# Performance work log

Hardware: AMD Instinct MI355X
Metric: run time of the kernel (lower is better)

The kernel has to match this reference:

```python
import jax, jax.numpy as jnp
import numpy as np
from jax import lax

SIM_THRESH = 0.9
MOTION_SCALE = 0.5
SALIENCY_SCALE = 0.5
EPS = 1e-6


def setup_inputs() -> dict:
    key = jax.random.key(0)
    k1, k2, k3, k4 = jax.random.split(key, 4)
    B, N, D, H, W = 128, 196, 768, 14, 14
    return {
        "tokens": jax.random.normal(k1, (B, N, D), dtype=jnp.float32),
        "motion_magnitude": jax.random.uniform(k2, (B, 1, H, W), dtype=jnp.float32),
        "saliency_map": jax.random.uniform(k3, (B, 1, H, W), dtype=jnp.float32),
        "compression_ratio": jax.random.uniform(k4, (B, H, W), dtype=jnp.float32),
    }


def _importance(motion, saliency, ratio):
    # motion/saliency are already (B,1,14,14) == (height,width), so
    # adaptive_avg_pool2d to (14,14) is the identity.
    B = motion.shape[0]
    m = motion.reshape(B, -1)
    m = m / (jnp.max(m) + EPS)               # global max, as in torch .max()
    s = saliency.reshape(B, -1)
    s = s / (jnp.max(s) + EPS)
    r = ratio.reshape(B, -1)
    imp = (MOTION_SCALE * m + SALIENCY_SCALE * s
           + (1.0 - MOTION_SCALE - SALIENCY_SCALE) * r)
    lo = imp.min(axis=1, keepdims=True)
    hi = imp.max(axis=1, keepdims=True)
    return (imp - lo) / (hi - lo + EPS)      # (B, N)


def _groups(adj):
    """Sequential BFS grouping over roots, faithful to the torch loop.

    adj: bool (N,N) directed edge mask. Returns (group_ids int32 (N,), num_groups).
    """
    N = adj.shape[0]

    def root_step(carry, r):
        assigned, gids, gid = carry

        def assign(c):
            assigned, gids, gid = c
            # BFS from root r, only through currently-unassigned nodes
            allowed = (~assigned).at[r].set(True)
            reach0 = jnp.zeros(N, dtype=bool).at[r].set(True)

            def body(s):
                reach, _ = s
                nxt = reach | (jnp.any(adj & reach[:, None], axis=0) & allowed)
                return nxt, jnp.any(nxt != reach)

            reach, _ = lax.while_loop(lambda s: s[1], body, (reach0, True))
            return assigned | reach, jnp.where(reach, gid, gids), gid + 1

        carry = lax.cond(assigned[r], lambda c: c, assign, carry)
        return carry, None

    init = (jnp.zeros(N, dtype=bool), jnp.zeros(N, dtype=jnp.int32), jnp.int32(0))
    (_, gids, ngroups), _ = lax.scan(root_step, init, jnp.arange(N))
    return gids, ngroups


def _merge_one(tokens_b, imp_b, adj_b):
    N = tokens_b.shape[0]
    gids, ng = _groups(adj_b)
    denom = jax.ops.segment_sum(imp_b, gids, num_segments=N) + EPS
    w = imp_b / denom[gids]
    merged = jax.ops.segment_sum(tokens_b * w[:, None], gids, num_segments=N)
    return merged, gids, ng


def reference(tokens, motion_magnitude, saliency_map, compression_ratio):
    B, N, D = tokens.shape
    imp = _importance(motion_magnitude, saliency_map, compression_ratio)  # (B,N)

    # cosine similarity (F.normalize with eps=1e-12)
    norm = jnp.maximum(jnp.linalg.norm(tokens, axis=-1, keepdims=True), 1e-12)
    tn = tokens / norm
    sim = jnp.einsum('bnd,bmd->bnm', tn, tn)
    sim = sim * (1.0 - jnp.eye(N, dtype=sim.dtype))  # zero diagonal

    # directed merge mask: similarity * (1 - importance_row)
    mask = (sim > SIM_THRESH).astype(sim.dtype) * (1.0 - imp[:, :, None])
    adj = mask > 0.5

    merged, gids, ng = jax.vmap(_merge_one)(tokens, imp, adj)
    # merged padded to N groups (rows >= num_groups are zero)
    return merged, sim, imp, gids
```

## Files before the change

kernel.cpp:

```cpp
#include <hip/hip_runtime.h>
#include <cstdint>

static constexpr int cB = 128;
static constexpr int cN = 196;
static constexpr int cD = 768;
static constexpr int cNN = cN * cN;
static constexpr int cND = cN * cD;
static constexpr float cEPS = 1e-6f;
static constexpr size_t cBND = (size_t)cB * cN * cD;

typedef __attribute__((ext_vector_type(8))) short short8;
typedef __attribute__((ext_vector_type(8))) unsigned short u16x8;
typedef __attribute__((ext_vector_type(4))) float f32x4;
typedef unsigned long long u64;

__device__ __forceinline__ unsigned short bf16_rne(float x) {
    unsigned u = __builtin_bit_cast(unsigned, x);
    u += 0x7FFFu + ((u >> 16) & 1u);
    return (unsigned short)(u >> 16);
}

__global__ __launch_bounds__(256) void k_imp(const float* __restrict__ mo,
                                             const float* __restrict__ sa,
                                             float* __restrict__ out_imp,
                                             float* __restrict__ ws_imp,
                                             float* __restrict__ ws_w,
                                             u64* __restrict__ ws_adj) {
    int b = blockIdx.x, t = threadIdx.x;
    __shared__ float redm[4], reds[4], lo_s[4], hi_s[4], MS[2], LOHI[2];

    for (int i = b * 256 + t; i < cB * cN * 4; i += cB * 256) ws_adj[i] = 0ull;

    const float4* mo4 = (const float4*)mo;
    const float4* sa4 = (const float4*)sa;
    float mm = 0.f, ms = 0.f;
    for (int i = t; i < cB * cN / 4; i += 256) {
        float4 a = mo4[i], c = sa4[i];
        mm = fmaxf(mm, fmaxf(fmaxf(a.x, a.y), fmaxf(a.z, a.w)));
        ms = fmaxf(ms, fmaxf(fmaxf(c.x, c.y), fmaxf(c.z, c.w)));
    }
    #pragma unroll
    for (int off = 32; off; off >>= 1) {
        mm = fmaxf(mm, __shfl_down(mm, off));
        ms = fmaxf(ms, __shfl_down(ms, off));
    }
    if ((t & 63) == 0) { redm[t >> 6] = mm; reds[t >> 6] = ms; }
    __syncthreads();
    if (t == 0) {
        float a = redm[0], c = reds[0];
        for (int w = 1; w < 4; w++) { a = fmaxf(a, redm[w]); c = fmaxf(c, reds[w]); }
        MS[0] = 1.0f / (a + cEPS);
        MS[1] = 1.0f / (c + cEPS);
    }
    __syncthreads();
    float Minv = MS[0], Sinv = MS[1];
    float v = 0.f, lo = 1e30f, hi = -1e30f;
    if (t < cN) {
        v = 0.5f * mo[b * cN + t] * Minv + 0.5f * sa[b * cN + t] * Sinv;
        lo = v; hi = v;
    }
    #pragma unroll
    for (int off = 32; off; off >>= 1) {
        lo = fminf(lo, __shfl_down(lo, off));
        hi = fmaxf(hi, __shfl_down(hi, off));
    }
    if ((t & 63) == 0) { lo_s[t >> 6] = lo; hi_s[t >> 6] = hi; }
    __syncthreads();
    if (t == 0) {
        float l = lo_s[0], h = hi_s[0];
        for (int w = 1; w < 4; w++) { l = fminf(l, lo_s[w]); h = fmaxf(h, hi_s[w]); }
        LOHI[0] = l; LOHI[1] = h;
    }
    __syncthreads();
    if (t < cN) {
        float imp = (v - LOHI[0]) / (LOHI[1] - LOHI[0] + cEPS);
        out_imp[b * cN + t] = imp;
        ws_imp[b * cN + t] = imp;
        ws_w[b * cN + t] = imp / (imp + cEPS);
    }
}

__global__ __launch_bounds__(256) void k_prep(const float* __restrict__ tok,
                                              const float* __restrict__ ws_w,
                                              float* __restrict__ ws_invn,
                                              float* __restrict__ merged) {
    int t = threadIdx.x;
    int tk = blockIdx.x * 8 + (t >> 5);
    int l  = t & 31;
    const float4* src = (const float4*)(tok + (size_t)tk * cD) + l;
    float4* dst = (float4*)(merged + (size_t)tk * cD) + l;
    float w = ws_w[tk];
    float4 v[6];
    #pragma unroll
    for (int j = 0; j < 6; j++) v[j] = src[32 * j];
    float s = 0.f;
    #pragma unroll
    for (int j = 0; j < 6; j++) {
        float4 x = v[j];
        s += x.x * x.x + x.y * x.y + x.z * x.z + x.w * x.w;
        dst[32 * j] = make_float4(x.x * w, x.y * w, x.z * w, x.w * w);
    }
    s += __shfl_xor(s, 1);  s += __shfl_xor(s, 2);
    s += __shfl_xor(s, 4);  s += __shfl_xor(s, 8);
    s += __shfl_xor(s, 16);
    if (l == 0) ws_invn[tk] = 1.0f / fmaxf(sqrtf(s), 1e-12f);
}

__global__ __launch_bounds__(256, 2) void k_sim(const float* __restrict__ tok,
                                                const float* __restrict__ ws_invn,
                                                const float* __restrict__ ws_imp,
                                                float* __restrict__ out_sim,
                                                u64* __restrict__ ws_adj) {
    __shared__ unsigned short sA[128 * 40];
    __shared__ unsigned short sB[128 * 40];
    __shared__ float invR[128], invC[128], impR[128], impC[128];
    __shared__ u64 ldsAdj[256];
    __shared__ u64 ldsAdjT[256];

    int bid = blockIdx.x;
    int xcd = bid & 7;
    int lin = bid >> 3;
    int b   = xcd + 8 * (lin / 3);
    int tc  = lin % 3;
    int rb = (tc == 2) ? 128 : 0;
    int cb = (tc == 0) ? 0 : 128;
    bool diag = (tc != 1);

    int t = threadIdx.x;
    int w = t >> 6, lane = t & 63;
    int lr = lane & 15, kf = (lane >> 4) * 8;
    int wr = (w >> 1) * 64, wc = (w & 1) * 64;
    const size_t bN = (size_t)b * cN;
    const float* tb = tok + bN * cD;

    ldsAdj[t] = 0ull;
    ldsAdjT[t] = 0ull;
    if (t < 128) {
        int gr = rb + t;
        invR[t] = (gr < cN) ? ws_invn[bN + gr] : 0.f;
        impR[t] = (gr < cN) ? ws_imp[bN + gr] : 1.f;
    } else {
        int gc = cb + (t - 128);
        invC[t - 128] = (gc < cN) ? ws_invn[bN + gc] : 0.f;
        impC[t - 128] = (gc < cN) ? ws_imp[bN + gc] : 1.f;
    }

    f32x4 acc[4][4];
    #pragma unroll
    for (int i = 0; i < 4; i++)
        #pragma unroll
        for (int j = 0; j < 4; j++) acc[i][j] = (f32x4){0.f, 0.f, 0.f, 0.f};

    int srow = t >> 2;
    int q = t & 3;

    float4 bufA[8], bufB[8];

    auto LOADS = [&](int k0, float4 (&r)[8]) {
        int koff = k0 + 8 * q;
        #pragma unroll
        for (int p = 0; p < 2; ++p) {
            int row = srow + 64 * p;
            float4 z = make_float4(0.f, 0.f, 0.f, 0.f);
            r[2 * p] = z; r[2 * p + 1] = z;
            int gr = rb + row;
            if (gr < cN) {
                const float4* pa = (const float4*)(tb + (size_t)gr * cD + koff);
                r[2 * p] = pa[0]; r[2 * p + 1] = pa[1];
            }
            if (!diag) {
                r[4 + 2 * p] = z; r[4 + 2 * p + 1] = z;
                int gc = cb + row;
                if (gc < cN) {
                    const float4* pb = (const float4*)(tb + (size_t)gc * cD + koff);
                    r[4 + 2 * p] = pb[0]; r[4 + 2 * p + 1] = pb[1];
                }
            }
        }
    };
    auto PACK = [&](const float4 (&r)[8]) {
        #pragma unroll
        for (int p = 0; p < 2; ++p) {
            int row = srow + 64 * p;
            float4 a0 = r[2 * p], a1 = r[2 * p + 1];
            u16x8 ha;
            ha[0] = bf16_rne(a0.x); ha[1] = bf16_rne(a0.y);
            ha[2] = bf16_rne(a0.z); ha[3] = bf16_rne(a0.w);
            ha[4] = bf16_rne(a1.x); ha[5] = bf16_rne(a1.y);
            ha[6] = bf16_rne(a1.z); ha[7] = bf16_rne(a1.w);
            *(u16x8*)&sA[row * 40 + 8 * q] = ha;
            if (!diag) {
                float4 b0 = r[4 + 2 * p], b1 = r[4 + 2 * p + 1];
                u16x8 hb;
                hb[0] = bf16_rne(b0.x); hb[1] = bf16_rne(b0.y);
                hb[2] = bf16_rne(b0.z); hb[3] = bf16_rne(b0.w);
                hb[4] = bf16_rne(b1.x); hb[5] = bf16_rne(b1.y);
                hb[6] = bf16_rne(b1.z); hb[7] = bf16_rne(b1.w);
                *(u16x8*)&sB[row * 40 + 8 * q] = hb;
            }
        }
    };
    auto COMPUTE = [&]() {
        short8 af[4], bf[4];
        #pragma unroll
        for (int rg = 0; rg < 4; rg++)
            af[rg] = *(const short8*)&sA[(wr + 16 * rg + lr) * 40 + kf];
        const unsigned short* sS = diag ? sA : sB;
        #pragma unroll
        for (int cg = 0; cg < 4; cg++)
            bf[cg] = *(const short8*)&sS[(wc + 16 * cg + lr) * 40 + kf];
        #pragma unroll
        for (int rg = 0; rg < 4; rg++)
            #pragma unroll
            for (int cg = 0; cg < 4; cg++)
                acc[rg][cg] = __builtin_amdgcn_mfma_f32_16x16x32_bf16(
                    af[rg], bf[cg], acc[rg][cg], 0, 0, 0);
    };

    LOADS(0, bufA);
    for (int k0 = 0; k0 < cD; k0 += 64) {
        PACK(bufA);
        __syncthreads();
        LOADS(k0 + 32, bufB);
        COMPUTE();
        __syncthreads();

        PACK(bufB);
        __syncthreads();
        if (k0 + 64 < cD) LOADS(k0 + 64, bufA);
        COMPUTE();
        __syncthreads();
    }

    float* so = out_sim + (size_t)b * cNN;
    int wloc = w >> 1;
    #pragma unroll
    for (int rg = 0; rg < 4; rg++) {
        int rBaseLoc = wr + 16 * rg + (lane >> 4) * 4;
        #pragma unroll
        for (int cg = 0; cg < 4; cg++) {
            int cLoc = wc + 16 * cg + lr;
            int C = cb + cLoc;
            if (C >= cN) continue;
            float ic = invC[cLoc];
            float imC = impC[cLoc];
            u64 bits = 0ull;
            #pragma unroll
            for (int i = 0; i < 4; i++) {
                int rLoc = rBaseLoc + i;
                int R = rb + rLoc;
                if (R >= cN) continue;
                float val = (R == C) ? 0.f : acc[rg][cg][i] * invR[rLoc] * ic;
                so[(size_t)R * cN + C] = val;
                if (val > 0.9f && impR[rLoc] < 0.5f) bits |= 1ull << (R & 63);
                if (!diag) {
                    so[(size_t)C * cN + R] = val;
                    if (val > 0.9f && imC < 0.5f)
                        atomicOr(&ldsAdjT[rLoc * 2 + ((C >> 6) & 1)],
                                 1ull << (C & 63));
                }
            }
            if (bits) atomicOr(&ldsAdj[cLoc * 2 + wloc], bits);
        }
    }
    __syncthreads();
    {
        int cLoc = t >> 1, wl = t & 1;
        int C = cb + cLoc;
        u64 v = ldsAdj[t];
        if (C < cN && v)
            atomicOr(&ws_adj[((size_t)b * cN + C) * 4 + (rb >> 6) + wl], v);
        if (!diag) {
            u64 vt = ldsAdjT[t];
            if (vt)
                atomicOr(&ws_adj[((size_t)b * cN + cLoc) * 4 + 2 + wl], vt);
        }
    }
}

__global__ __launch_bounds__(256) void k_group(const u64* __restrict__ ws_adj,
                                               const float* __restrict__ ws_imp,
                                               const float* __restrict__ tok,
                                               float* __restrict__ out_gids,
                                               float* __restrict__ ws_w,
                                               int* __restrict__ ws_flag,
                                               int* __restrict__ ws_gids,
                                               float* __restrict__ merged) {
    int b = blockIdx.x, t = threadIdx.x;
    __shared__ float impL[cN];
    __shared__ u64 reachw[4], assignedw[4], edge_s[4];
    __shared__ int flag;
    __shared__ int gidsL[cN];
    __shared__ float denomL[cN];
    __shared__ float wL[cN];

    u64 m0 = 0, m1 = 0, m2 = 0, m3 = 0;
    if (t < cN) {
        impL[t] = ws_imp[b * cN + t];
        const u64* ap = ws_adj + ((size_t)b * cN + t) * 4;
        m0 = ap[0]; m1 = ap[1]; m2 = ap[2]; m3 = ap[3];
    }
    u64 anym = m0 | m1 | m2 | m3;
    u64 bal = __ballot(anym != 0ull);
    if ((t & 63) == 0) edge_s[t >> 6] = bal;
    __syncthreads();
    bool has_edges = (edge_s[0] | edge_s[1] | edge_s[2] | edge_s[3]) != 0ull;

    if (!has_edges) {
        if (t < cN) {
            float imp = impL[t];
            ws_w[b * cN + t] = imp / (imp + cEPS);
            ws_gids[b * cN + t] = t;
            out_gids[b * cN + t] = (float)t;
        }
        if (t == 0) ws_flag[b] = 1;
        return;
    }

    if (t < 4) assignedw[t] = 0ull;
    if (t < cN) { gidsL[t] = 0; denomL[t] = 0.f; }
    __syncthreads();
    int gid = 0;
    int wrd_t = t >> 6, bit_t = t & 63;
    for (int r = 0; r < cN; r++) {
        if ((assignedw[r >> 6] >> (r & 63)) & 1ull) continue;
        if (t < 4) reachw[t] = (t == (r >> 6)) ? (1ull << (r & 63)) : 0ull;
        __syncthreads();
        int changed = 1;
        while (changed) {
            u64 hit = (m0 & reachw[0]) | (m1 & reachw[1]) |
                      (m2 & reachw[2]) | (m3 & reachw[3]);
            bool inre = (t < cN) && ((reachw[wrd_t] >> bit_t) & 1ull);
            bool unass = (t < cN) && !((assignedw[wrd_t] >> bit_t) & 1ull);
            bool p = inre || (hit != 0ull && unass);
            u64 nw = __ballot(p);
            __syncthreads();
            if (t == 0) flag = 0;
            __syncthreads();
            if ((t & 63) == 0) {
                if (nw != reachw[t >> 6]) flag = 1;
                reachw[t >> 6] = nw;
            }
            __syncthreads();
            changed = flag;
        }
        if ((t < cN) && ((reachw[wrd_t] >> bit_t) & 1ull)) gidsL[t] = gid;
        if (t < 4) assignedw[t] |= reachw[t];
        gid++;
        __syncthreads();
    }
    if (t < cN) atomicAdd(&denomL[gidsL[t]], impL[t]);
    __syncthreads();
    if (t < cN) {
        int g = gidsL[t];
        float wv = impL[t] / (denomL[g] + cEPS);
        ws_w[b * cN + t] = wv;
        wL[t] = wv;
        ws_gids[b * cN + t] = g;
        out_gids[b * cN + t] = (float)g;
    }
    if (t == 0) ws_flag[b] = 0;
    __syncthreads();

    if (t < 192) {
        for (int n = 0; n < cN; n++) {
            float4 acc = make_float4(0.f, 0.f, 0.f, 0.f);
            for (int j = 0; j < cN; j++) {
                if (gidsL[j] == n) {
                    const float4 v = *(const float4*)(tok + (size_t)b * cND + (size_t)j * cD + 4 * t);
                    float wv = wL[j];
                    acc.x += v.x * wv; acc.y += v.y * wv;
                    acc.z += v.z * wv; acc.w += v.w * wv;
                }
            }
            *(float4*)(merged + (size_t)b * cND + (size_t)n * cD + 4 * t) = acc;
        }
    }
}

extern "C" void kernel_launch(void* const* d_in, const int* in_sizes, int n_in,
                              void* d_out, int out_size, void* d_ws, size_t ws_size,
                              hipStream_t stream) {
    const float* tok = (const float*)d_in[0];
    const float* mo  = (const float*)d_in[1];
    const float* sa  = (const float*)d_in[2];

    float* out = (float*)d_out;
    float* out_merged = out;
    float* out_sim    = out + cBND;
    float* out_imp    = out_sim + (size_t)cB * cNN;
    float* out_gids   = out_imp + (size_t)cB * cN;

    u64*   ws_adj  = (u64*)d_ws;
    float* ws_imp  = (float*)(ws_adj + (size_t)cB * cN * 4);
    float* ws_w    = ws_imp + cB * cN;
    float* ws_invn = ws_w + cB * cN;
    int*   ws_flag = (int*)(ws_invn + cB * cN);
    int*   ws_gids = ws_flag + cB;

    k_imp<<<cB, 256, 0, stream>>>(mo, sa, out_imp, ws_imp, ws_w, ws_adj);
    k_prep<<<cB * cN / 8, 256, 0, stream>>>(tok, ws_w, ws_invn, out_merged);
    k_sim<<<384, 256, 0, stream>>>(tok, ws_invn, ws_imp, out_sim, ws_adj);
    k_group<<<cB, 256, 0, stream>>>(ws_adj, ws_imp, tok, out_gids, ws_w,
                                    ws_flag, ws_gids, out_merged);
}
```

Measured before the change: 212.5 us.

## Fuse norm computation and merged-token init into similarity kernel

Removes the separate k_prep kernel. Its work of computing per-token inverse norms and writing the weighted token copy into merged now happens inside k_sim's PACK stage, using the fp32 values already loaded for the bf16 GEMM tiles. The diagonal tiles write merged rows and reduce the squared sums with shuffles and shared memory before the epilogue. This saves one full read of the tokens tensor and one launch, but adds stores and an extra sync to the GEMM kernel, which could slow its pipeline.

```diff
diff --git a/kernel.cpp b/kernel.cpp
--- a/kernel.cpp
+++ b/kernel.cpp
@@ -80,37 +80,12 @@
     }
 }
 
-__global__ __launch_bounds__(256) void k_prep(const float* __restrict__ tok,
-                                              const float* __restrict__ ws_w,
-                                              float* __restrict__ ws_invn,
-                                              float* __restrict__ merged) {
-    int t = threadIdx.x;
-    int tk = blockIdx.x * 8 + (t >> 5);
-    int l  = t & 31;
-    const float4* src = (const float4*)(tok + (size_t)tk * cD) + l;
-    float4* dst = (float4*)(merged + (size_t)tk * cD) + l;
-    float w = ws_w[tk];
-    float4 v[6];
-    #pragma unroll
-    for (int j = 0; j < 6; j++) v[j] = src[32 * j];
-    float s = 0.f;
-    #pragma unroll
-    for (int j = 0; j < 6; j++) {
-        float4 x = v[j];
-        s += x.x * x.x + x.y * x.y + x.z * x.z + x.w * x.w;
-        dst[32 * j] = make_float4(x.x * w, x.y * w, x.z * w, x.w * w);
-    }
-    s += __shfl_xor(s, 1);  s += __shfl_xor(s, 2);
-    s += __shfl_xor(s, 4);  s += __shfl_xor(s, 8);
-    s += __shfl_xor(s, 16);
-    if (l == 0) ws_invn[tk] = 1.0f / fmaxf(sqrtf(s), 1e-12f);
-}
-
 __global__ __launch_bounds__(256, 2) void k_sim(const float* __restrict__ tok,
-                                                const float* __restrict__ ws_invn,
+                                                const float* __restrict__ ws_w,
                                                 const float* __restrict__ ws_imp,
                                                 float* __restrict__ out_sim,
-                                                u64* __restrict__ ws_adj) {
+                                                u64* __restrict__ ws_adj,
+                                                float* __restrict__ merged) {
     __shared__ unsigned short sA[128 * 40];
     __shared__ unsigned short sB[128 * 40];
     __shared__ float invR[128], invC[128], impR[128], impC[128];
@@ -132,16 +107,15 @@
     int wr = (w >> 1) * 64, wc = (w & 1) * 64;
     const size_t bN = (size_t)b * cN;
     const float* tb = tok + bN * cD;
+    float* mg = merged + bN * cD;
 
     ldsAdj[t] = 0ull;
     ldsAdjT[t] = 0ull;
     if (t < 128) {
         int gr = rb + t;
-        invR[t] = (gr < cN) ? ws_invn[bN + gr] : 0.f;
         impR[t] = (gr < cN) ? ws_imp[bN + gr] : 1.f;
     } else {
         int gc = cb + (t - 128);
-        invC[t - 128] = (gc < cN) ? ws_invn[bN + gc] : 0.f;
         impC[t - 128] = (gc < cN) ? ws_imp[bN + gc] : 1.f;
     }
 
@@ -153,6 +127,14 @@
 
     int srow = t >> 2;
     int q = t & 3;
+
+    float wA0 = 0.f, wA1 = 0.f;
+    if (diag) {
+        int g0 = rb + srow, g1 = rb + srow + 64;
+        if (g0 < cN) wA0 = ws_w[bN + g0];
+        if (g1 < cN) wA1 = ws_w[bN + g1];
+    }
+    float sa0 = 0.f, sa1 = 0.f, sb0 = 0.f, sb1 = 0.f;
 
     float4 bufA[8], bufB[8];
 
@@ -178,19 +160,34 @@
             }
         }
     };
-    auto PACK = [&](const float4 (&r)[8]) {
+    auto PACK = [&](const float4 (&r)[8], int k0p) {
+        int koff = k0p + 8 * q;
         #pragma unroll
         for (int p = 0; p < 2; ++p) {
             int row = srow + 64 * p;
             float4 a0 = r[2 * p], a1 = r[2 * p + 1];
+            float ds = a0.x * a0.x + a0.y * a0.y + a0.z * a0.z + a0.w * a0.w
+                     + a1.x * a1.x + a1.y * a1.y + a1.z * a1.z + a1.w * a1.w;
+            if (p) sa1 += ds; else sa0 += ds;
             u16x8 ha;
             ha[0] = bf16_rne(a0.x); ha[1] = bf16_rne(a0.y);
             ha[2] = bf16_rne(a0.z); ha[3] = bf16_rne(a0.w);
             ha[4] = bf16_rne(a1.x); ha[5] = bf16_rne(a1.y);
             ha[6] = bf16_rne(a1.z); ha[7] = bf16_rne(a1.w);
             *(u16x8*)&sA[row * 40 + 8 * q] = ha;
-            if (!diag) {
+            if (diag) {
+                int gr = rb + row;
+                if (gr < cN) {
+                    float wv = p ? wA1 : wA0;
+                    float4* md = (float4*)(mg + (size_t)gr * cD + koff);
+                    md[0] = make_float4(a0.x * wv, a0.y * wv, a0.z * wv, a0.w * wv);
+                    md[1] = make_float4(a1.x * wv, a1.y * wv, a1.z * wv, a1.w * wv);
+                }
+            } else {
                 float4 b0 = r[4 + 2 * p], b1 = r[4 + 2 * p + 1];
+                float dsb = b0.x * b0.x + b0.y * b0.y + b0.z * b0.z + b0.w * b0.w
+                          + b1.x * b1.x + b1.y * b1.y + b1.z * b1.z + b1.w * b1.w;
+                if (p) sb1 += dsb; else sb0 += dsb;
                 u16x8 hb;
                 hb[0] = bf16_rne(b0.x); hb[1] = bf16_rne(b0.y);
                 hb[2] = bf16_rne(b0.z); hb[3] = bf16_rne(b0.w);
@@ -219,18 +216,34 @@
 
     LOADS(0, bufA);
     for (int k0 = 0; k0 < cD; k0 += 64) {
-        PACK(bufA);
+        PACK(bufA, k0);
         __syncthreads();
         LOADS(k0 + 32, bufB);
         COMPUTE();
         __syncthreads();
 
-        PACK(bufB);
+        PACK(bufB, k0 + 32);
         __syncthreads();
         if (k0 + 64 < cD) LOADS(k0 + 64, bufA);
         COMPUTE();
         __syncthreads();
     }
+
+    sa0 += __shfl_xor(sa0, 1); sa0 += __shfl_xor(sa0, 2);
+    sa1 += __shfl_xor(sa1, 1); sa1 += __shfl_xor(sa1, 2);
+    if (!diag) {
+        sb0 += __shfl_xor(sb0, 1); sb0 += __shfl_xor(sb0, 2);
+        sb1 += __shfl_xor(sb1, 1); sb1 += __shfl_xor(sb1, 2);
+    }
+    if (q == 0) {
+        invR[srow] = sa0; invR[srow + 64] = sa1;
+        if (diag) { invC[srow] = sa0; invC[srow + 64] = sa1; }
+        else      { invC[srow] = sb0; invC[srow + 64] = sb1; }
+    }
+    __syncthreads();
+    if (t < 128) invR[t] = 1.0f / fmaxf(sqrtf(invR[t]), 1e-12f);
+    else { int c = t - 128; invC[c] = 1.0f / fmaxf(sqrtf(invC[c]), 1e-12f); }
+    __syncthreads();
 
     float* so = out_sim + (size_t)b * cNN;
     int wloc = w >> 1;
@@ -394,13 +407,11 @@
     u64*   ws_adj  = (u64*)d_ws;
     float* ws_imp  = (float*)(ws_adj + (size_t)cB * cN * 4);
     float* ws_w    = ws_imp + cB * cN;
-    float* ws_invn = ws_w + cB * cN;
-    int*   ws_flag = (int*)(ws_invn + cB * cN);
+    int*   ws_flag = (int*)(ws_w + cB * cN);
     int*   ws_gids = ws_flag + cB;
 
     k_imp<<<cB, 256, 0, stream>>>(mo, sa, out_imp, ws_imp, ws_w, ws_adj);
-    k_prep<<<cB * cN / 8, 256, 0, stream>>>(tok, ws_w, ws_invn, out_merged);
-    k_sim<<<384, 256, 0, stream>>>(tok, ws_invn, ws_imp, out_sim, ws_adj);
+    k_sim<<<384, 256, 0, stream>>>(tok, ws_w, ws_imp, out_sim, ws_adj, out_merged);
     k_group<<<cB, 256, 0, stream>>>(ws_adj, ws_imp, tok, out_gids, ws_w,
                                     ws_flag, ws_gids, out_merged);
 }
```

Measured after the change: 198.3 us. 1.07x faster.
